# Kernel optimization log

Hardware: AMD Instinct MI355X
Metric: run time of the kernel (lower is better)

Reference implementation:

```python
import jax, jax.numpy as jnp
import numpy as np

N, H, E, ED = 50000, 128, 600000, 32
LN_EPS = 1e-5


def _mlp(x, W1, b1, W2, b2):
    h = jax.nn.gelu(x @ W1 + b1, approximate=False)
    return h @ W2 + b2


def setup_inputs() -> dict:
    key = jax.random.key(0)
    ks = jax.random.split(key, 12)
    s = lambda fan_in: 1.0 / np.sqrt(fan_in)
    return {
        "x": jax.random.normal(ks[0], (N, H), dtype=jnp.float32),
        "edge_index": jax.random.randint(ks[1], (2, E), 0, N, dtype=jnp.int64),
        "edge_attr": jax.random.normal(ks[2], (E, ED), dtype=jnp.float32),
        "eW1": jax.random.normal(ks[3], (2 * H + ED, H), dtype=jnp.float32) * s(2 * H + ED),
        "eb1": jnp.zeros((H,), dtype=jnp.float32),
        "eW2": jax.random.normal(ks[4], (H, H), dtype=jnp.float32) * s(H),
        "eb2": jnp.zeros((H,), dtype=jnp.float32),
        "nW1": jax.random.normal(ks[5], (2 * H, H), dtype=jnp.float32) * s(2 * H),
        "nb1": jnp.zeros((H,), dtype=jnp.float32),
        "nW2": jax.random.normal(ks[6], (H, H), dtype=jnp.float32) * s(H),
        "nb2": jnp.zeros((H,), dtype=jnp.float32),
        "ln_g": jnp.ones((H,), dtype=jnp.float32),
        "ln_b": jnp.zeros((H,), dtype=jnp.float32),
    }


def reference(x, edge_index, edge_attr, eW1, eb1, eW2, eb2, nW1, nb1, nW2, nb2, ln_g, ln_b):
    src, dst = edge_index[0], edge_index[1]
    # edge MLP on gathered endpoint features + edge attrs: [E, 2H+ED] -> [E, H]
    msg = _mlp(jnp.concatenate([x[src], x[dst], edge_attr], axis=-1), eW1, eb1, eW2, eb2)
    # scatter-mean into destination nodes
    agg = jax.ops.segment_sum(msg, dst, num_segments=x.shape[0])
    count = jax.ops.segment_sum(jnp.ones((dst.shape[0], 1), dtype=x.dtype), dst, num_segments=x.shape[0])
    agg = agg / (count + 1e-8)
    # node MLP + residual + layernorm
    out = _mlp(jnp.concatenate([x, agg], axis=-1), nW1, nb1, nW2, nb2) + x
    mu = jnp.mean(out, axis=-1, keepdims=True)
    var = jnp.mean(jnp.square(out - mu), axis=-1, keepdims=True)
    return (out - mu) * jax.lax.rsqrt(var + LN_EPS) * ln_g + ln_b
```

## Files before the change

### kernel.cpp

```cpp
#include <hip/hip_runtime.h>
#include <hip/hip_fp16.h>
#include <math.h>

#define NN 50000
#define HH 128
#define EE 600000
#define EDD 32
#define NBINS 50176
#define NPRE 782
#define NHIST 586
#define NWG_E (EE / 64)

typedef __attribute__((ext_vector_type(8))) _Float16 half8;
typedef __attribute__((ext_vector_type(4))) float f32x4;

__device__ __forceinline__ unsigned pkh(float a, float b) {
  __half2 h = __floats2half2_rn(a, b);
  return *reinterpret_cast<unsigned*>(&h);
}
__device__ __forceinline__ unsigned hadd2u(unsigned a, unsigned b) {
  __half2 x = *reinterpret_cast<__half2*>(&a);
  __half2 y = *reinterpret_cast<__half2*>(&b);
  __half2 s = __hadd2(x, y);
  return *reinterpret_cast<unsigned*>(&s);
}
__device__ __forceinline__ unsigned hmul2u(unsigned a, unsigned b) {
  __half2 x = *reinterpret_cast<__half2*>(&a);
  __half2 y = *reinterpret_cast<__half2*>(&b);
  __half2 s = __hmul2(x, y);
  return *reinterpret_cast<unsigned*>(&s);
}
__device__ __forceinline__ short f2hs(float f) {
  __half h = __float2half_rn(f);
  return *reinterpret_cast<short*>(&h);
}
__device__ __forceinline__ float h2f(short s) {
  __half h = *reinterpret_cast<__half*>(&s);
  return __half2float(h);
}

__device__ __forceinline__ float gelu_f(float v) {
  float u = v * fmaf(0.10294324f, v * v, 2.3022082f);
  float e = __builtin_amdgcn_exp2f(u);
  float r = __builtin_amdgcn_rcpf(e + 1.0f);
  return fmaf(-v, r, v);
}

__device__ __forceinline__ __half2 gelu2(__half2 v) {
  const __half2 c2 = __floats2half2_rn(0.10294324f, 0.10294324f);
  const __half2 K2 = __floats2half2_rn(2.3022082f, 2.3022082f);
  const __half2 one2 = __floats2half2_rn(1.0f, 1.0f);
  __half2 t = __hmul2(v, v);
  __half2 p = __hfma2(t, c2, K2);
  __half2 u = __hmul2(v, p);
  __half2 e = __halves2half2(hexp2(__low2half(u)), hexp2(__high2half(u)));
  __half2 d = __hadd2(e, one2);
  __half2 r = __halves2half2(hrcp(__low2half(d)), hrcp(__high2half(d)));
  return __hfma2(__hneg2(v), r, v);
}

#define FS 132
__global__ __launch_bounds__(256) void k_setup(
    const float* __restrict__ eW1, const float* __restrict__ nW1,
    const float* __restrict__ nW2, const float* __restrict__ eW2,
    const float* __restrict__ eb2, const long long* __restrict__ ei,
    long long nmax,
    short* __restrict__ pe1, short* __restrict__ pn1, short* __restrict__ pn2,
    short* __restrict__ pnW2p, float* __restrict__ b2p,
    int* __restrict__ zbase, int* __restrict__ flag) {
  __shared__ short sA[64 * 136];
  __shared__ float sR[64 * FS];
  __shared__ int bad;
  const int blk = blockIdx.x;
  const int tid = threadIdx.x;

  if (blk < 42) {
    const int b = blk * 4 + (tid >> 6);
    const int l = tid & 63;
    const float* W;
    short* P;
    int bb;
    if (b < 72)       { W = eW1; P = pe1; bb = b; }
    else if (b < 136) { W = nW1; P = pn1; bb = b - 72; }
    else              { W = nW2; P = pn2; bb = b - 136; }
    const int kt = bb >> 3, ct = bb & 7;
    short v[8];
#pragma unroll
    for (int j = 0; j < 8; ++j)
      v[j] = f2hs(W[(size_t)(kt * 32 + ((l >> 4) * 8 + j)) * HH + ct * 16 + (l & 15)]);
    short* dst = P + ((size_t)bb * 64 + l) * 8;
#pragma unroll
    for (int j = 0; j < 8; ++j) dst[j] = v[j];
    return;
  }
  if (blk == 42) {
    if (tid == 0) bad = 0;
    __syncthreads();
    for (int i = tid; i < 2048; i += 256) {
      long long v = ei[i];
      if (v < 0 || v >= nmax) bad = 1;
    }
    __syncthreads();
    if (tid == 0) *flag = (bad ? 0 : 1);
    return;
  }
  if (blk < 92) {
    int idx = (blk - 43) * 2048 + tid * 8;
    int4 z = {0, 0, 0, 0};
    *(int4*)(zbase + idx) = z;
    *(int4*)(zbase + idx + 4) = z;
    return;
  }
  if (blk == 94) {
    if (tid < 128) {
      float acc = 0.f;
#pragma unroll 4
      for (int k = 0; k < 128; ++k)
        acc += eb2[k] * nW1[(size_t)(128 + k) * HH + tid];
      b2p[tid] = acc;
    }
    return;
  }
  {
    const int b = blk - 92;
    const int le = tid >> 2, lq = tid & 3;
    const int wv = tid >> 6, l = tid & 63, lr = l & 15, kq = l >> 4;

    half8 bf[8];
#pragma unroll
    for (int kt = 0; kt < 4; ++kt)
#pragma unroll
      for (int c = 0; c < 2; ++c) {
        half8 v;
#pragma unroll
        for (int j = 0; j < 8; ++j)
          v[j] = (_Float16)nW1[(size_t)(128 + kt * 32 + ((l >> 4) * 8 + j)) * HH +
                               (wv * 2 + c) * 16 + (l & 15)];
        bf[kt * 2 + c] = v;
      }
    {
      const float4* xs = (const float4*)(eW2 + (size_t)(64 * b + le) * HH);
#pragma unroll
      for (int i = 0; i < 4; ++i) {
        float4 a = xs[lq * 8 + i * 2], c = xs[lq * 8 + i * 2 + 1];
        uint4 u = {pkh(a.x, a.y), pkh(a.z, a.w), pkh(c.x, c.y), pkh(c.z, c.w)};
        *(uint4*)&sA[le * 136 + lq * 32 + i * 8] = u;
      }
    }
    __syncthreads();

    f32x4 acc[4][2];
    const f32x4 zero = {0.f, 0.f, 0.f, 0.f};
#pragma unroll
    for (int m = 0; m < 4; ++m) { acc[m][0] = zero; acc[m][1] = zero; }
    const short* ab = &sA[lr * 136 + kq * 8];
#pragma unroll
    for (int kt = 0; kt < 4; ++kt) {
      half8 af[4];
#pragma unroll
      for (int m = 0; m < 4; ++m) af[m] = *(const half8*)(ab + m * 16 * 136 + kt * 32);
#pragma unroll
      for (int m = 0; m < 4; ++m)
#pragma unroll
        for (int c = 0; c < 2; ++c)
          acc[m][c] = __builtin_amdgcn_mfma_f32_16x16x32_f16(af[m], bf[kt * 2 + c], acc[m][c], 0, 0, 0);
    }
#pragma unroll
    for (int c = 0; c < 2; ++c)
#pragma unroll
      for (int m = 0; m < 4; ++m)
#pragma unroll
        for (int r = 0; r < 4; ++r)
          sR[(m * 16 + kq * 4 + r) * FS + wv * 32 + c * 16 + lr] = acc[m][c][r];
    __syncthreads();

#pragma unroll
    for (int it = 0; it < 4; ++it) {
      int item = tid + 256 * it;
      int lane = item & 63;
      int pair = item >> 6;
      int ktl = pair >> 3, ct = pair & 7;
      short v[8];
#pragma unroll
      for (int j = 0; j < 8; ++j) {
        int kpos = ktl * 32 + ((lane >> 4) * 8 + j);
        int t2 = kpos >> 1, h2 = kpos & 1;
        int rowl = (t2 >> 4) * 32 + (t2 & 15) + 16 * h2;
        int colp = ct * 16 + (lane & 15);
        v[j] = f2hs(sR[rowl * FS + colp]);
      }
      short* dst = pnW2p + (((size_t)(2 * b + ktl) * 8 + ct) * 64 + lane) * 8;
#pragma unroll
      for (int j = 0; j < 8; ++j) dst[j] = v[j];
    }
  }
}

__global__ __launch_bounds__(256, 4) void k_preh(
    const float* __restrict__ x, const short* __restrict__ pW1,
    const float* __restrict__ eb1,
    const void* __restrict__ eiv, const int* __restrict__ flag,
    unsigned* __restrict__ Psw, unsigned* __restrict__ Pdw,
    unsigned* __restrict__ HaggH2, int* __restrict__ chist) {
  __shared__ short sX[64 * 136];
  const int blk = blockIdx.x;
  const int tid = threadIdx.x;

  if (blk >= NPRE) {
    int base = ((blk - NPRE) * 256 + tid) * 4;
    if (*flag) {
      const long long* p = (const long long*)eiv + EE;
#pragma unroll
      for (int j = 0; j < 4; ++j) {
        int e = base + j;
        if (e < EE) atomicAdd(&chist[(int)p[e]], 1);
      }
    } else {
      const int* p = (const int*)eiv + EE;
      if (base + 3 < EE) {
        int4 d4 = *(const int4*)(p + base);
        atomicAdd(&chist[d4.x], 1);
        atomicAdd(&chist[d4.y], 1);
        atomicAdd(&chist[d4.z], 1);
        atomicAdd(&chist[d4.w], 1);
      } else {
        for (int j = 0; j < 4; ++j) {
          int e = base + j;
          if (e < EE) atomicAdd(&chist[p[e]], 1);
        }
      }
    }
    return;
  }

  const int r0 = blk * 64;
  const int le = tid >> 2, lq = tid & 3;
  const int wv = tid >> 6, l = tid & 63, lr = l & 15, kq = l >> 4;

  {
    int gr = r0 + le;
    if (gr < NN) {
      uint4 z = {0, 0, 0, 0};
      uint4* hp = (uint4*)(HaggH2 + (size_t)gr * 64);
#pragma unroll
      for (int i = 0; i < 4; ++i) hp[lq * 4 + i] = z;
    }
  }

  const float b1c0 = eb1[wv * 32 + lr];
  const float b1c1 = eb1[wv * 32 + 16 + lr];

  const half8* bp = (const half8*)pW1;
  half8 fa[8], fb[8];
#pragma unroll
  for (int kt = 0; kt < 4; ++kt)
#pragma unroll
    for (int c = 0; c < 2; ++c) {
      fa[kt * 2 + c] = bp[(kt * 8 + wv * 2 + c) * 64 + l];
      fb[kt * 2 + c] = bp[((kt + 4) * 8 + wv * 2 + c) * 64 + l];
    }
  {
    int gr = r0 + le;
    if (gr < NN) {
      const float4* xs = (const float4*)(x + (size_t)gr * HH);
#pragma unroll
      for (int i = 0; i < 4; ++i) {
        float4 a = xs[lq * 8 + i * 2], c = xs[lq * 8 + i * 2 + 1];
        uint4 u = {pkh(a.x, a.y), pkh(a.z, a.w), pkh(c.x, c.y), pkh(c.z, c.w)};
        *(uint4*)&sX[le * 136 + lq * 32 + i * 8] = u;
      }
    } else {
      uint4 z = {0, 0, 0, 0};
#pragma unroll
      for (int i = 0; i < 4; ++i) *(uint4*)&sX[le * 136 + lq * 32 + i * 8] = z;
    }
  }
  __syncthreads();

  f32x4 as_[4][2], ad[4][2];
  const f32x4 zero = {0.f, 0.f, 0.f, 0.f};
#pragma unroll
  for (int m = 0; m < 4; ++m) { as_[m][0] = zero; as_[m][1] = zero; ad[m][0] = zero; ad[m][1] = zero; }
  const short* ab = &sX[lr * 136 + kq * 8];
#pragma unroll
  for (int kt = 0; kt < 4; ++kt) {
    half8 af[4];
#pragma unroll
    for (int m = 0; m < 4; ++m) af[m] = *(const half8*)(ab + m * 16 * 136 + kt * 32);
#pragma unroll
    for (int m = 0; m < 4; ++m)
#pragma unroll
      for (int c = 0; c < 2; ++c) {
        as_[m][c] = __builtin_amdgcn_mfma_f32_16x16x32_f16(af[m], fa[kt * 2 + c], as_[m][c], 0, 0, 0);
        ad[m][c] = __builtin_amdgcn_mfma_f32_16x16x32_f16(af[m], fb[kt * 2 + c], ad[m][c], 0, 0, 0);
      }
  }
#pragma unroll
  for (int m = 0; m < 4; ++m)
#pragma unroll
    for (int r = 0; r < 4; ++r) {
      int grow = r0 + m * 16 + kq * 4 + r;
      if (grow < NN) {
        Psw[(size_t)grow * 64 + wv * 16 + lr] =
            pkh(as_[m][0][r] + b1c0, as_[m][1][r] + b1c1);
        Pdw[(size_t)grow * 64 + wv * 16 + lr] = pkh(ad[m][0][r], ad[m][1][r]);
      }
    }
}

__global__ void k_scan1(const int* __restrict__ chist, int* __restrict__ tmp,
                        int* __restrict__ bsum) {
  __shared__ int buf[2][256];
  int t = threadIdx.x;
  int i = blockIdx.x * 256 + t;
  int self = chist[i];
  buf[0][t] = self;
  __syncthreads();
  int cur = 0;
  for (int o = 1; o < 256; o <<= 1) {
    int v = buf[cur][t];
    if (t >= o) v += buf[cur][t - o];
    buf[cur ^ 1][t] = v;
    __syncthreads();
    cur ^= 1;
  }
  tmp[i] = buf[cur][t] - self;
  if (t == 255) bsum[blockIdx.x] = buf[cur][255];
}

__global__ void k_scatter(const void* __restrict__ eiv, const int* __restrict__ flag,
                          const int* __restrict__ tmp,
                          const int* __restrict__ bsum, int* __restrict__ cntW,
                          unsigned long long* __restrict__ e8) {
  __shared__ int sB[2][256];
  const int t = threadIdx.x;
  int orig = (t < 196) ? bsum[t] : 0;
  sB[0][t] = orig;
  __syncthreads();
  int cur = 0;
  for (int o = 1; o < 256; o <<= 1) {
    int v = sB[cur][t];
    if (t >= o) v += sB[cur][t - o];
    sB[cur ^ 1][t] = v;
    __syncthreads();
    cur ^= 1;
  }
  sB[1][t] = sB[0][t] - orig;
  __syncthreads();

  int e = blockIdx.x * 256 + t;
  if (e >= EE) return;
  int s, d;
  if (*flag) {
    const long long* p = (const long long*)eiv;
    s = (int)p[e];
    d = (int)p[EE + e];
  } else {
    const int* p = (const int*)eiv;
    s = p[e];
    d = p[EE + e];
  }
  int base = tmp[d] + sB[1][d >> 8];
  int pos = base + atomicAdd(&cntW[d], 1);
  e8[pos] = (unsigned long long)s | ((unsigned long long)d << 20) |
            ((unsigned long long)e << 40);
}

#define SFP 68
__global__ __launch_bounds__(256, 7) void k_edge(
    const unsigned* __restrict__ Psw, const unsigned* __restrict__ Pdw,
    const float* __restrict__ ea,
    const short* __restrict__ pW1,
    const unsigned long long* __restrict__ e8, unsigned* __restrict__ HaggH2) {
  __shared__ unsigned sFp[64 * SFP];
  __shared__ short sEA[64 * 40];
  __shared__ int sDst[64];

  int orig = blockIdx.x;
  const int q8 = NWG_E >> 3, r8 = NWG_E & 7;
  int xcd = orig & 7, lid = orig >> 3;
  int swz = (xcd < r8) ? xcd * (q8 + 1) + lid
                       : r8 * (q8 + 1) + (xcd - r8) * q8 + lid;

  const int tid = threadIdx.x;
  const int e0 = swz * 64;
  const int le = tid >> 2, lq = tid & 3;
  const int wv = tid >> 6, l = tid & 63, lr = l & 15, kq = l >> 4;

  half8 w1c[2];
#pragma unroll
  for (int c = 0; c < 2; ++c)
    w1c[c] = ((const half8*)pW1)[(64 + wv * 2 + c) * 64 + l];

  const unsigned long long er = e8[e0 + le];
  const int gs = (int)(er & 0xFFFFF);
  const int gd = (int)((er >> 20) & 0xFFFFF);
  const int ge = (int)(er >> 40);
  if (lq == 0) sDst[le] = gd;

  {
    const uint4* ps = (const uint4*)(Psw + (size_t)gs * 64);
    const uint4* pd = (const uint4*)(Pdw + (size_t)gd * 64);
#pragma unroll
    for (int i = 0; i < 4; ++i) {
      uint4 a = ps[lq * 4 + i];
      uint4 b = pd[lq * 4 + i];
      uint4 s = {hadd2u(a.x, b.x), hadd2u(a.y, b.y), hadd2u(a.z, b.z), hadd2u(a.w, b.w)};
      *(uint4*)&sFp[le * SFP + lq * 16 + i * 4] = s;
    }
    const float4* ep = (const float4*)(ea + (size_t)ge * EDD);
    float4 a = ep[lq * 2], b = ep[lq * 2 + 1];
    uint4 u = {pkh(a.x, a.y), pkh(a.z, a.w), pkh(b.x, b.y), pkh(b.z, b.w)};
    *(uint4*)&sEA[le * 40 + lq * 8] = u;
  }
  __syncthreads();

  f32x4 acc[4][2];
  const f32x4 zero = {0.f, 0.f, 0.f, 0.f};
#pragma unroll
  for (int m = 0; m < 4; ++m) { acc[m][0] = zero; acc[m][1] = zero; }
  {
#pragma unroll
    for (int m = 0; m < 4; ++m) {
      half8 af = *(const half8*)&sEA[(m * 16 + lr) * 40 + kq * 8];
#pragma unroll
      for (int c = 0; c < 2; ++c)
        acc[m][c] = __builtin_amdgcn_mfma_f32_16x16x32_f16(af, w1c[c], acc[m][c], 0, 0, 0);
    }
  }

  unsigned pr[4][4];
#pragma unroll
  for (int m = 0; m < 4; ++m)
#pragma unroll
    for (int r = 0; r < 4; ++r) {
      const int row = m * 16 + kq * 4 + r;
      unsigned up = sFp[row * SFP + wv * 16 + lr];
      __half2 P = *reinterpret_cast<__half2*>(&up);
      __half2 v = __hadd2(__floats2half2_rn(acc[m][0][r], acc[m][1][r]), P);
      __half2 hg = gelu2(v);
      pr[m][r] = *reinterpret_cast<unsigned*>(&hg);
    }
  __syncthreads();

  {
    unsigned* tp = &sFp[(wv * 16 + lr) * SFP];
#pragma unroll
    for (int m = 0; m < 4; ++m) {
      uint4 u = {pr[m][0], pr[m][1], pr[m][2], pr[m][3]};
      *(uint4*)&tp[m * 16 + kq * 4] = u;
    }
  }
  __syncthreads();

  {
    const int p = tid & 63;
    const int q = tid >> 6;
    const unsigned* tp2 = &sFp[p * SFP + q * 16];
    const int rend = q * 16 + 15;
    __half2 run = __floats2half2_rn(0.f, 0.f);
#pragma unroll
    for (int i = 0; i < 4; ++i) {
      uint4 u4 = *(const uint4*)&tp2[i * 4];
      unsigned uu[4] = {u4.x, u4.y, u4.z, u4.w};
#pragma unroll
      for (int j = 0; j < 4; ++j) {
        int r = q * 16 + i * 4 + j;
        run = __hadd2(run, *reinterpret_cast<__half2*>(&uu[j]));
        int dcur = sDst[r];
        bool last = (r == rend) || (sDst[r + 1] != dcur);
        if (last) {
          unsafeAtomicAdd((__half2*)&HaggH2[(size_t)dcur * 64 + p], run);
          run = __floats2half2_rn(0.f, 0.f);
        }
      }
    }
  }
}

#define NS 264
__global__ __launch_bounds__(256, 4) void k_node(
    const float* __restrict__ x,
    const unsigned* __restrict__ HaggH2, const int* __restrict__ chist,
    const short* __restrict__ pn1, const short* __restrict__ pnW2p,
    const float* __restrict__ nb1, const float* __restrict__ b2p,
    const short* __restrict__ pn2, const float* __restrict__ nb2,
    const float* __restrict__ g, const float* __restrict__ be,
    float* __restrict__ out) {
  __shared__ short sA[64 * NS];
  __shared__ float sP[64 * 4];
  __shared__ float sP2[64 * 4];
  __shared__ float sFac[64];

  const int tid = threadIdx.x;
  const int r0 = blockIdx.x * 64;
  const int le = tid >> 2;
  const int lq = tid & 3;
  const int wv = tid >> 6;
  const int l = tid & 63;
  const int lr = l & 15;
  const int kq = l >> 4;

  const half8* bpa = (const half8*)pn1;
  const half8* bpc = (const half8*)pnW2p;
  half8 b1f[16];
#pragma unroll
  for (int kt = 0; kt < 4; ++kt)
#pragma unroll
    for (int c = 0; c < 2; ++c) {
      b1f[kt * 2 + c] = bpa[(kt * 8 + wv * 2 + c) * 64 + l];
      b1f[(kt + 4) * 2 + c] = bpc[(kt * 8 + wv * 2 + c) * 64 + l];
    }

  {
    const int gr = r0 + le;
    short* row = &sA[le * NS];
    if (gr < NN) {
      float cntf = (float)chist[gr];
      float rinv = 1.0f / (cntf + 1e-8f);
      if (lq == 0) sFac[le] = cntf * rinv;
      const float4* xs = (const float4*)(x + (size_t)gr * HH);
#pragma unroll
      for (int i = 0; i < 4; ++i) {
        float4 a = xs[lq * 8 + i * 2], c = xs[lq * 8 + i * 2 + 1];
        uint4 u = {pkh(a.x, a.y), pkh(a.z, a.w), pkh(c.x, c.y), pkh(c.z, c.w)};
        *(uint4*)(row + lq * 32 + i * 8) = u;
      }
      const unsigned rv2 = pkh(rinv, rinv);
      const uint4* hs = (const uint4*)(HaggH2 + (size_t)gr * 64);
#pragma unroll
      for (int i = 0; i < 4; ++i) {
        uint4 u = hs[lq * 4 + i];
        u.x = hmul2u(u.x, rv2);
        u.y = hmul2u(u.y, rv2);
        u.z = hmul2u(u.z, rv2);
        u.w = hmul2u(u.w, rv2);
        *(uint4*)(row + 128 + lq * 32 + i * 8) = u;
      }
    } else {
      if (lq == 0) sFac[le] = 0.f;
      uint4 z = {0, 0, 0, 0};
#pragma unroll
      for (int i = 0; i < 8; ++i) *(uint4*)(row + lq * 64 + i * 8) = z;
    }
  }
  __syncthreads();

  f32x4 acc[4][2];
  const f32x4 zero = {0.f, 0.f, 0.f, 0.f};
#pragma unroll
  for (int m = 0; m < 4; ++m) { acc[m][0] = zero; acc[m][1] = zero; }
  const short* ab = &sA[lr * NS + kq * 8];
#pragma unroll
  for (int kt = 0; kt < 8; ++kt) {
    half8 af[4];
#pragma unroll
    for (int m = 0; m < 4; ++m)
      af[m] = *(const half8*)(ab + m * 16 * NS + kt * 32);
#pragma unroll
    for (int m = 0; m < 4; ++m)
#pragma unroll
      for (int c = 0; c < 2; ++c)
        acc[m][c] = __builtin_amdgcn_mfma_f32_16x16x32_f16(af[m], b1f[kt * 2 + c], acc[m][c], 0, 0, 0);
  }

  const half8* bp2 = (const half8*)pn2;
  half8 b2f_[8];
#pragma unroll
  for (int kt = 0; kt < 4; ++kt)
#pragma unroll
    for (int c = 0; c < 2; ++c)
      b2f_[kt * 2 + c] = bp2[(kt * 8 + wv * 2 + c) * 64 + l];

  __syncthreads();

#pragma unroll
  for (int c = 0; c < 2; ++c) {
    const int col = wv * 32 + c * 16 + lr;
    const float b1v = nb1[col];
    const float b2pv = b2p[col];
#pragma unroll
    for (int m = 0; m < 4; ++m)
#pragma unroll
      for (int r = 0; r < 4; ++r) {
        const int row = m * 16 + kq * 4 + r;
        float fac = sFac[row];
        sA[row * NS + 128 + col] = f2hs(gelu_f(acc[m][c][r] + b1v + fac * b2pv));
      }
  }
  __syncthreads();

  f32x4 acc2[4][2];
#pragma unroll
  for (int m = 0; m < 4; ++m) { acc2[m][0] = zero; acc2[m][1] = zero; }
#pragma unroll
  for (int kt = 0; kt < 4; ++kt) {
    half8 af[4];
#pragma unroll
    for (int m = 0; m < 4; ++m)
      af[m] = *(const half8*)(ab + m * 16 * NS + 128 + kt * 32);
#pragma unroll
    for (int m = 0; m < 4; ++m)
#pragma unroll
      for (int c = 0; c < 2; ++c)
        acc2[m][c] = __builtin_amdgcn_mfma_f32_16x16x32_f16(af[m], b2f_[kt * 2 + c], acc2[m][c], 0, 0, 0);
  }

  float val[4][2][4];
#pragma unroll
  for (int c = 0; c < 2; ++c) {
    const int col = wv * 32 + c * 16 + lr;
    const float b2v = nb2[col];
#pragma unroll
    for (int m = 0; m < 4; ++m)
#pragma unroll
      for (int r = 0; r < 4; ++r) {
        const int lrow = m * 16 + kq * 4 + r;
        float xr = h2f(sA[lrow * NS + col]);
        val[m][c][r] = acc2[m][c][r] + b2v + xr;
      }
  }
#pragma unroll
  for (int m = 0; m < 4; ++m)
#pragma unroll
    for (int r = 0; r < 4; ++r) {
      float s = val[m][0][r] + val[m][1][r];
      float s2 = val[m][0][r] * val[m][0][r] + val[m][1][r] * val[m][1][r];
#pragma unroll
      for (int o = 1; o < 16; o <<= 1) {
        s += __shfl_xor(s, o);
        s2 += __shfl_xor(s2, o);
      }
      if (lr == 0) {
        const int row = m * 16 + kq * 4 + r;
        sP[row * 4 + wv] = s;
        sP2[row * 4 + wv] = s2;
      }
    }
  __syncthreads();

#pragma unroll
  for (int c = 0; c < 2; ++c) {
    const int col = wv * 32 + c * 16 + lr;
    const float gv = g[col];
    const float bv = be[col];
#pragma unroll
    for (int m = 0; m < 4; ++m)
#pragma unroll
      for (int r = 0; r < 4; ++r) {
        const int lrow = m * 16 + kq * 4 + r;
        const int row = r0 + lrow;
        if (row < NN) {
          float4 ps = *(float4*)&sP[lrow * 4];
          float4 qs = *(float4*)&sP2[lrow * 4];
          float s = ps.x + ps.y + ps.z + ps.w;
          float s2 = qs.x + qs.y + qs.z + qs.w;
          float mu = s * 0.0078125f;
          float var = s2 * 0.0078125f - mu * mu;
          float rs = rsqrtf(var + 1e-5f);
          out[(size_t)row * HH + col] = (val[m][c][r] - mu) * rs * gv + bv;
        }
      }
  }
}

extern "C" void kernel_launch(void* const* d_in, const int* in_sizes, int n_in,
                              void* d_out, int out_size, void* d_ws, size_t ws_size,
                              hipStream_t stream) {
  const float* x = (const float*)d_in[0];
  const void* ei = d_in[1];
  const float* ea = (const float*)d_in[2];
  const float* eW1 = (const float*)d_in[3];
  const float* eb1 = (const float*)d_in[4];
  const float* eW2 = (const float*)d_in[5];
  const float* eb2 = (const float*)d_in[6];
  const float* nW1 = (const float*)d_in[7];
  const float* nb1 = (const float*)d_in[8];
  const float* nW2 = (const float*)d_in[9];
  const float* nb2 = (const float*)d_in[10];
  const float* lng = (const float*)d_in[11];
  const float* lnb = (const float*)d_in[12];
  float* out = (float*)d_out;

  char* w = (char*)d_ws;
  size_t off = 0;
  auto alloc = [&](size_t bytes) { void* p = w + off; off = (off + bytes + 255) & ~(size_t)255; return p; };
  unsigned* HaggH2 = (unsigned*)alloc((size_t)NN * 64 * 4);
  int* chist = (int*)alloc((size_t)NBINS * 4);
  int* cntW = (int*)alloc((size_t)NBINS * 4);
  short* pe1 = (short*)alloc((size_t)72 * 512 * 2);
  short* pn1 = (short*)alloc((size_t)64 * 512 * 2);
  short* pn2 = (short*)alloc((size_t)32 * 512 * 2);
  short* pnW2p = (short*)alloc((size_t)32 * 512 * 2);
  float* b2p = (float*)alloc(HH * 4);
  unsigned long long* e8 = (unsigned long long*)alloc((size_t)EE * 8);
  int* tmpS = (int*)alloc((size_t)NBINS * 4);
  int* bsum = (int*)alloc(256 * 4);
  int* flag = (int*)alloc(256);
  unsigned* Psw = (unsigned*)alloc((size_t)NN * 64 * 4);
  unsigned* Pdw = (unsigned*)alloc((size_t)NN * 64 * 4);

  k_setup<<<95, 256, 0, stream>>>(eW1, nW1, nW2, eW2, eb2, (const long long*)ei,
                                  (long long)NN, pe1, pn1, pn2, pnW2p, b2p, chist, flag);
  k_preh<<<NPRE + NHIST, 256, 0, stream>>>(x, pe1, eb1, ei, flag, Psw, Pdw, HaggH2, chist);
  k_scan1<<<NBINS / 256, 256, 0, stream>>>(chist, tmpS, bsum);
  k_scatter<<<(EE + 255) / 256, 256, 0, stream>>>(ei, flag, tmpS, bsum, cntW, e8);
  k_edge<<<NWG_E, 256, 0, stream>>>(Psw, Pdw, ea, pe1, e8, HaggH2);
  k_node<<<(NN + 63) / 64, 256, 0, stream>>>(x, HaggH2, chist, pn1, pnW2p, nb1, b2p, pn2, nb2, lng, lnb, out);
}
```

Before: 152.9 us.

## Rebalance pipeline stages, merge scan into preh, swizzle edge LDS, use wave shuffles

The destination histogram moves into k_setup, with each block re-checking the index width locally, and the block-level scan moves into k_preh. This removes the separate k_scan1 launch and the zeroing blocks, which are replaced by hipMemsetAsync. In k_edge the padded LDS arrays become XOR-swizzled uint4 arrays, and the shared destination array is replaced by __shfl and __ballot. Less LDS lets occupancy rise from 7 to 8 blocks. The memset adds an API call, and every histogram block now repeats the index-width check.

Result: slower. 158.2 us (+3.4%).

```diff
diff --git a/kernel.cpp b/kernel.cpp
--- a/kernel.cpp
+++ b/kernel.cpp
@@ -67,13 +67,47 @@
     long long nmax,
     short* __restrict__ pe1, short* __restrict__ pn1, short* __restrict__ pn2,
     short* __restrict__ pnW2p, float* __restrict__ b2p,
-    int* __restrict__ zbase, int* __restrict__ flag) {
+    int* __restrict__ chist, int* __restrict__ flag) {
   __shared__ short sA[64 * 136];
   __shared__ float sR[64 * FS];
   __shared__ int bad;
   const int blk = blockIdx.x;
   const int tid = threadIdx.x;
 
+  if (blk >= 46) {
+    if (tid == 0) bad = 0;
+    __syncthreads();
+    {
+      long long v = ei[tid];
+      if (v < 0 || v >= nmax) bad = 1;
+    }
+    __syncthreads();
+    const int isL = !bad;
+    int base = ((blk - 46) * 256 + tid) * 4;
+    if (isL) {
+      const long long* p = ei + EE;
+#pragma unroll
+      for (int j = 0; j < 4; ++j) {
+        int e = base + j;
+        if (e < EE) atomicAdd(&chist[(int)p[e]], 1);
+      }
+    } else {
+      const int* p = (const int*)ei + EE;
+      if (base + 3 < EE) {
+        int4 d4 = *(const int4*)(p + base);
+        atomicAdd(&chist[d4.x], 1);
+        atomicAdd(&chist[d4.y], 1);
+        atomicAdd(&chist[d4.z], 1);
+        atomicAdd(&chist[d4.w], 1);
+      } else {
+        for (int j = 0; j < 4; ++j) {
+          int e = base + j;
+          if (e < EE) atomicAdd(&chist[p[e]], 1);
+        }
+      }
+    }
+    return;
+  }
   if (blk < 42) {
     const int b = blk * 4 + (tid >> 6);
     const int l = tid & 63;
@@ -104,14 +138,7 @@
     if (tid == 0) *flag = (bad ? 0 : 1);
     return;
   }
-  if (blk < 92) {
-    int idx = (blk - 43) * 2048 + tid * 8;
-    int4 z = {0, 0, 0, 0};
-    *(int4*)(zbase + idx) = z;
-    *(int4*)(zbase + idx + 4) = z;
-    return;
-  }
-  if (blk == 94) {
+  if (blk == 45) {
     if (tid < 128) {
       float acc = 0.f;
 #pragma unroll 4
@@ -122,7 +149,7 @@
     return;
   }
   {
-    const int b = blk - 92;
+    const int b = blk - 43;
     const int le = tid >> 2, lq = tid & 3;
     const int wv = tid >> 6, l = tid & 63, lr = l & 15, kq = l >> 4;
 
@@ -199,37 +226,30 @@
 __global__ __launch_bounds__(256, 4) void k_preh(
     const float* __restrict__ x, const short* __restrict__ pW1,
     const float* __restrict__ eb1,
-    const void* __restrict__ eiv, const int* __restrict__ flag,
     unsigned* __restrict__ Psw, unsigned* __restrict__ Pdw,
-    unsigned* __restrict__ HaggH2, int* __restrict__ chist) {
+    unsigned* __restrict__ HaggH2,
+    const int* __restrict__ chist, int* __restrict__ tmp, int* __restrict__ bsum) {
   __shared__ short sX[64 * 136];
+  __shared__ int buf[2][256];
   const int blk = blockIdx.x;
   const int tid = threadIdx.x;
 
   if (blk >= NPRE) {
-    int base = ((blk - NPRE) * 256 + tid) * 4;
-    if (*flag) {
-      const long long* p = (const long long*)eiv + EE;
-#pragma unroll
-      for (int j = 0; j < 4; ++j) {
-        int e = base + j;
-        if (e < EE) atomicAdd(&chist[(int)p[e]], 1);
-      }
-    } else {
-      const int* p = (const int*)eiv + EE;
-      if (base + 3 < EE) {
-        int4 d4 = *(const int4*)(p + base);
-        atomicAdd(&chist[d4.x], 1);
-        atomicAdd(&chist[d4.y], 1);
-        atomicAdd(&chist[d4.z], 1);
-        atomicAdd(&chist[d4.w], 1);
-      } else {
-        for (int j = 0; j < 4; ++j) {
-          int e = base + j;
-          if (e < EE) atomicAdd(&chist[p[e]], 1);
-        }
-      }
-    }
+    int sb = blk - NPRE;
+    int i = sb * 256 + tid;
+    int self = chist[i];
+    buf[0][tid] = self;
+    __syncthreads();
+    int cur = 0;
+    for (int o = 1; o < 256; o <<= 1) {
+      int v = buf[cur][tid];
+      if (tid >= o) v += buf[cur][tid - o];
+      buf[cur ^ 1][tid] = v;
+      __syncthreads();
+      cur ^= 1;
+    }
+    tmp[i] = buf[cur][tid] - self;
+    if (tid == 255) bsum[sb] = buf[cur][255];
     return;
   }
 
@@ -306,26 +326,6 @@
         Pdw[(size_t)grow * 64 + wv * 16 + lr] = pkh(ad[m][0][r], ad[m][1][r]);
       }
     }
-}
-
-__global__ void k_scan1(const int* __restrict__ chist, int* __restrict__ tmp,
-                        int* __restrict__ bsum) {
-  __shared__ int buf[2][256];
-  int t = threadIdx.x;
-  int i = blockIdx.x * 256 + t;
-  int self = chist[i];
-  buf[0][t] = self;
-  __syncthreads();
-  int cur = 0;
-  for (int o = 1; o < 256; o <<= 1) {
-    int v = buf[cur][t];
-    if (t >= o) v += buf[cur][t - o];
-    buf[cur ^ 1][t] = v;
-    __syncthreads();
-    cur ^= 1;
-  }
-  tmp[i] = buf[cur][t] - self;
-  if (t == 255) bsum[blockIdx.x] = buf[cur][255];
 }
 
 __global__ void k_scatter(const void* __restrict__ eiv, const int* __restrict__ flag,
@@ -366,15 +366,13 @@
             ((unsigned long long)e << 40);
 }
 
-#define SFP 68
-__global__ __launch_bounds__(256, 7) void k_edge(
+__global__ __launch_bounds__(256, 8) void k_edge(
     const unsigned* __restrict__ Psw, const unsigned* __restrict__ Pdw,
     const float* __restrict__ ea,
     const short* __restrict__ pW1,
     const unsigned long long* __restrict__ e8, unsigned* __restrict__ HaggH2) {
-  __shared__ unsigned sFp[64 * SFP];
-  __shared__ short sEA[64 * 40];
-  __shared__ int sDst[64];
+  __shared__ uint4 sFp4[64 * 16];
+  __shared__ uint4 sEA4[64 * 4];
 
   int orig = blockIdx.x;
   const int q8 = NWG_E >> 3, r8 = NWG_E & 7;
@@ -396,7 +394,6 @@
   const int gs = (int)(er & 0xFFFFF);
   const int gd = (int)((er >> 20) & 0xFFFFF);
   const int ge = (int)(er >> 40);
-  if (lq == 0) sDst[le] = gd;
 
   {
     const uint4* ps = (const uint4*)(Psw + (size_t)gs * 64);
@@ -406,12 +403,12 @@
       uint4 a = ps[lq * 4 + i];
       uint4 b = pd[lq * 4 + i];
       uint4 s = {hadd2u(a.x, b.x), hadd2u(a.y, b.y), hadd2u(a.z, b.z), hadd2u(a.w, b.w)};
-      *(uint4*)&sFp[le * SFP + lq * 16 + i * 4] = s;
+      sFp4[le * 16 + ((lq * 4 + i) ^ (le & 15))] = s;
     }
     const float4* ep = (const float4*)(ea + (size_t)ge * EDD);
     float4 a = ep[lq * 2], b = ep[lq * 2 + 1];
     uint4 u = {pkh(a.x, a.y), pkh(a.z, a.w), pkh(b.x, b.y), pkh(b.z, b.w)};
-    *(uint4*)&sEA[le * 40 + lq * 8] = u;
+    sEA4[le * 4 + (lq ^ (le & 3))] = u;
   }
   __syncthreads();
 
@@ -422,20 +419,24 @@
   {
 #pragma unroll
     for (int m = 0; m < 4; ++m) {
-      half8 af = *(const half8*)&sEA[(m * 16 + lr) * 40 + kq * 8];
+      uint4 av = sEA4[(m * 16 + lr) * 4 + (kq ^ (lr & 3))];
+      half8 af = *reinterpret_cast<half8*>(&av);
 #pragma unroll
       for (int c = 0; c < 2; ++c)
         acc[m][c] = __builtin_amdgcn_mfma_f32_16x16x32_f16(af, w1c[c], acc[m][c], 0, 0, 0);
     }
   }
 
+  const unsigned* sFpW = (const unsigned*)sFp4;
+  const int pairU4 = wv * 4 + (lr >> 2);
+  const int pairW = lr & 3;
   unsigned pr[4][4];
 #pragma unroll
   for (int m = 0; m < 4; ++m)
 #pragma unroll
     for (int r = 0; r < 4; ++r) {
       const int row = m * 16 + kq * 4 + r;
-      unsigned up = sFp[row * SFP + wv * 16 + lr];
+      unsigned up = sFpW[(row * 16 + (pairU4 ^ (row & 15))) * 4 + pairW];
       __half2 P = *reinterpret_cast<__half2*>(&up);
       __half2 v = __hadd2(__floats2half2_rn(acc[m][0][r], acc[m][1][r]), P);
       __half2 hg = gelu2(v);
@@ -444,11 +445,11 @@
   __syncthreads();
 
   {
-    unsigned* tp = &sFp[(wv * 16 + lr) * SFP];
+    const int pair = wv * 16 + lr;
 #pragma unroll
     for (int m = 0; m < 4; ++m) {
       uint4 u = {pr[m][0], pr[m][1], pr[m][2], pr[m][3]};
-      *(uint4*)&tp[m * 16 + kq * 4] = u;
+      sFp4[pair * 16 + ((m * 4 + kq) ^ lr)] = u;
     }
   }
   __syncthreads();
@@ -456,19 +457,19 @@
   {
     const int p = tid & 63;
     const int q = tid >> 6;
-    const unsigned* tp2 = &sFp[p * SFP + q * 16];
-    const int rend = q * 16 + 15;
+    int gnxt = __shfl_down(gd, 4, 64);
+    unsigned long long bmask = __ballot(gd != gnxt);
     __half2 run = __floats2half2_rn(0.f, 0.f);
 #pragma unroll
     for (int i = 0; i < 4; ++i) {
-      uint4 u4 = *(const uint4*)&tp2[i * 4];
+      uint4 u4 = sFp4[p * 16 + ((q * 4 + i) ^ (p & 15))];
       unsigned uu[4] = {u4.x, u4.y, u4.z, u4.w};
 #pragma unroll
       for (int j = 0; j < 4; ++j) {
-        int r = q * 16 + i * 4 + j;
+        const int jj = i * 4 + j;
         run = __hadd2(run, *reinterpret_cast<__half2*>(&uu[j]));
-        int dcur = sDst[r];
-        bool last = (r == rend) || (sDst[r + 1] != dcur);
+        int dcur = __shfl(gd, jj * 4, 64);
+        bool last = (jj == 15) || ((bmask >> (jj * 4)) & 1);
         if (last) {
           unsafeAtomicAdd((__half2*)&HaggH2[(size_t)dcur * 64 + p], run);
           run = __floats2half2_rn(0.f, 0.f);
@@ -700,10 +701,11 @@
   unsigned* Psw = (unsigned*)alloc((size_t)NN * 64 * 4);
   unsigned* Pdw = (unsigned*)alloc((size_t)NN * 64 * 4);
 
-  k_setup<<<95, 256, 0, stream>>>(eW1, nW1, nW2, eW2, eb2, (const long long*)ei,
-                                  (long long)NN, pe1, pn1, pn2, pnW2p, b2p, chist, flag);
-  k_preh<<<NPRE + NHIST, 256, 0, stream>>>(x, pe1, eb1, ei, flag, Psw, Pdw, HaggH2, chist);
-  k_scan1<<<NBINS / 256, 256, 0, stream>>>(chist, tmpS, bsum);
+  hipMemsetAsync(chist, 0, (size_t)NBINS * 4 * 2, stream);
+  k_setup<<<46 + NHIST, 256, 0, stream>>>(eW1, nW1, nW2, eW2, eb2,
+                                          (const long long*)ei, (long long)NN,
+                                          pe1, pn1, pn2, pnW2p, b2p, chist, flag);
+  k_preh<<<NPRE + 196, 256, 0, stream>>>(x, pe1, eb1, Psw, Pdw, HaggH2, chist, tmpS, bsum);
   k_scatter<<<(EE + 255) / 256, 256, 0, stream>>>(ei, flag, tmpS, bsum, cntW, e8);
   k_edge<<<NWG_E, 256, 0, stream>>>(Psw, Pdw, ea, pe1, e8, HaggH2);
   k_node<<<(NN + 63) / 64, 256, 0, stream>>>(x, HaggH2, chist, pn1, pnW2p, nb1, b2p, pn2, nb2, lng, lnb, out);
```

## Swizzle edge-kernel LDS layout and use wave shuffles for segment boundaries

Applied to the files above, without the earlier changes.

Replaces the padded shared-memory tiles in k_edge with XOR-swizzled uint4 layouts, removing the padding and aiming to avoid LDS bank conflicts on the fill, fragment-load and transpose passes. The per-edge destination array in LDS is dropped: destination ids and run boundaries now come from wave shuffles and a ballot mask over the per-thread gd values. The launch-bounds occupancy hint goes from 7 to 8 blocks per CU, which the smaller LDS footprint makes possible but which tightens the register budget. The swizzle index math adds ALU work and must stay consistent across all four access sites.

Result: no change. 152.7 us (-0.2%).

```diff
diff --git a/kernel.cpp b/kernel.cpp
--- a/kernel.cpp
+++ b/kernel.cpp
@@ -366,15 +366,13 @@
             ((unsigned long long)e << 40);
 }
 
-#define SFP 68
-__global__ __launch_bounds__(256, 7) void k_edge(
+__global__ __launch_bounds__(256, 8) void k_edge(
     const unsigned* __restrict__ Psw, const unsigned* __restrict__ Pdw,
     const float* __restrict__ ea,
     const short* __restrict__ pW1,
     const unsigned long long* __restrict__ e8, unsigned* __restrict__ HaggH2) {
-  __shared__ unsigned sFp[64 * SFP];
-  __shared__ short sEA[64 * 40];
-  __shared__ int sDst[64];
+  __shared__ uint4 sFp4[64 * 16];
+  __shared__ uint4 sEA4[64 * 4];
 
   int orig = blockIdx.x;
   const int q8 = NWG_E >> 3, r8 = NWG_E & 7;
@@ -396,7 +394,6 @@
   const int gs = (int)(er & 0xFFFFF);
   const int gd = (int)((er >> 20) & 0xFFFFF);
   const int ge = (int)(er >> 40);
-  if (lq == 0) sDst[le] = gd;
 
   {
     const uint4* ps = (const uint4*)(Psw + (size_t)gs * 64);
@@ -406,12 +403,12 @@
       uint4 a = ps[lq * 4 + i];
       uint4 b = pd[lq * 4 + i];
       uint4 s = {hadd2u(a.x, b.x), hadd2u(a.y, b.y), hadd2u(a.z, b.z), hadd2u(a.w, b.w)};
-      *(uint4*)&sFp[le * SFP + lq * 16 + i * 4] = s;
+      sFp4[le * 16 + ((lq * 4 + i) ^ (le & 15))] = s;
     }
     const float4* ep = (const float4*)(ea + (size_t)ge * EDD);
     float4 a = ep[lq * 2], b = ep[lq * 2 + 1];
     uint4 u = {pkh(a.x, a.y), pkh(a.z, a.w), pkh(b.x, b.y), pkh(b.z, b.w)};
-    *(uint4*)&sEA[le * 40 + lq * 8] = u;
+    sEA4[le * 4 + (lq ^ (le & 3))] = u;
   }
   __syncthreads();
 
@@ -422,20 +419,24 @@
   {
 #pragma unroll
     for (int m = 0; m < 4; ++m) {
-      half8 af = *(const half8*)&sEA[(m * 16 + lr) * 40 + kq * 8];
+      uint4 av = sEA4[(m * 16 + lr) * 4 + (kq ^ (lr & 3))];
+      half8 af = *reinterpret_cast<half8*>(&av);
 #pragma unroll
       for (int c = 0; c < 2; ++c)
         acc[m][c] = __builtin_amdgcn_mfma_f32_16x16x32_f16(af, w1c[c], acc[m][c], 0, 0, 0);
     }
   }
 
+  const unsigned* sFpW = (const unsigned*)sFp4;
+  const int pairU4 = wv * 4 + (lr >> 2);
+  const int pairW = lr & 3;
   unsigned pr[4][4];
 #pragma unroll
   for (int m = 0; m < 4; ++m)
 #pragma unroll
     for (int r = 0; r < 4; ++r) {
       const int row = m * 16 + kq * 4 + r;
-      unsigned up = sFp[row * SFP + wv * 16 + lr];
+      unsigned up = sFpW[(row * 16 + (pairU4 ^ (row & 15))) * 4 + pairW];
       __half2 P = *reinterpret_cast<__half2*>(&up);
       __half2 v = __hadd2(__floats2half2_rn(acc[m][0][r], acc[m][1][r]), P);
       __half2 hg = gelu2(v);
@@ -444,11 +445,11 @@
   __syncthreads();
 
   {
-    unsigned* tp = &sFp[(wv * 16 + lr) * SFP];
+    const int pair = wv * 16 + lr;
 #pragma unroll
     for (int m = 0; m < 4; ++m) {
       uint4 u = {pr[m][0], pr[m][1], pr[m][2], pr[m][3]};
-      *(uint4*)&tp[m * 16 + kq * 4] = u;
+      sFp4[pair * 16 + ((m * 4 + kq) ^ lr)] = u;
     }
   }
   __syncthreads();
@@ -456,19 +457,19 @@
   {
     const int p = tid & 63;
     const int q = tid >> 6;
-    const unsigned* tp2 = &sFp[p * SFP + q * 16];
-    const int rend = q * 16 + 15;
+    int gnxt = __shfl_down(gd, 4, 64);
+    unsigned long long bmask = __ballot(gd != gnxt);
     __half2 run = __floats2half2_rn(0.f, 0.f);
 #pragma unroll
     for (int i = 0; i < 4; ++i) {
-      uint4 u4 = *(const uint4*)&tp2[i * 4];
+      uint4 u4 = sFp4[p * 16 + ((q * 4 + i) ^ (p & 15))];
       unsigned uu[4] = {u4.x, u4.y, u4.z, u4.w};
 #pragma unroll
       for (int j = 0; j < 4; ++j) {
-        int r = q * 16 + i * 4 + j;
+        const int jj = i * 4 + j;
         run = __hadd2(run, *reinterpret_cast<__half2*>(&uu[j]));
-        int dcur = sDst[r];
-        bool last = (r == rend) || (sDst[r + 1] != dcur);
+        int dcur = __shfl(gd, jj * 4, 64);
+        bool last = (jj == 15) || ((bmask >> (jj * 4)) & 1);
         if (last) {
           unsafeAtomicAdd((__half2*)&HaggH2[(size_t)dcur * 64 + p], run);
           run = __floats2half2_rn(0.f, 0.f);
```
